# Kernel tuning notes

Hardware: AMD Instinct MI355X
Metric: run time of the kernel (lower is better)

The kernel has to match this reference:

```python
import jax, jax.numpy as jnp
import numpy as np

N_NODES = 50000
N_EDGES = 600000
N_RELS = 500
D = 128


def setup_inputs() -> dict:
    key = jax.random.key(0)
    ks = jax.random.split(key, 8)
    h = jax.random.normal(ks[0], (N_NODES, D), dtype=jnp.float32)
    norm = jax.random.uniform(ks[1], (N_NODES, 1), dtype=jnp.float32)
    rel_emb = jax.random.normal(ks[2], (N_RELS, D), dtype=jnp.float32)
    # xavier-uniform-like scale for square weights
    lim = np.sqrt(6.0 / (D + D)) * np.sqrt(2.0)
    W_neighbor = jax.random.uniform(ks[3], (D, D), dtype=jnp.float32, minval=-lim, maxval=lim)
    loop_weight = jax.random.uniform(ks[4], (D, D), dtype=jnp.float32, minval=-lim, maxval=lim)
    edge_src = jax.random.randint(ks[5], (N_EDGES,), 0, N_NODES, dtype=jnp.int64 if jax.config.jax_enable_x64 else jnp.int32)
    edge_dst = jax.random.randint(ks[6], (N_EDGES,), 0, N_NODES, dtype=edge_src.dtype)
    edge_type = jax.random.randint(ks[7], (N_EDGES,), 0, N_RELS, dtype=edge_src.dtype)
    return {
        "h": h, "norm": norm, "rel_emb": rel_emb,
        "W_neighbor": W_neighbor, "loop_weight": loop_weight,
        "edge_src": edge_src, "edge_dst": edge_dst, "edge_type": edge_type,
    }


def reference(h, norm, rel_emb, W_neighbor, loop_weight, edge_src, edge_dst, edge_type):
    # self-loop message (dense GEMM on node features)
    loop_message = h @ loop_weight  # [N, D]

    # msg_func: gather rel emb + src features, compose ('sub' branch computes node + relation
    # in the original source, reproduced faithfully), dense matmul per edge
    relation = rel_emb[edge_type]          # [E, D] gather
    node = h[edge_src]                     # [E, D] gather
    msg = (node + relation) @ W_neighbor   # [E, D]

    # fn.sum aggregate: scatter-sum messages into destination nodes
    agg = jax.ops.segment_sum(msg, edge_dst, num_segments=h.shape[0])  # [N, D]

    # apply_func: multiply by per-node norm
    node_repr = agg * norm  # [N, D]

    # self_loop add, then activation (relu); dropout=0.0 -> identity
    node_repr = jax.nn.relu(node_repr + loop_message)
    return node_repr
```

## Files before the change

kernel.cpp:

```cpp
#include <hip/hip_runtime.h>

#define NN 50000
#define NE 600000
#define NR 500
#define DD 128
#define CAP 64

#define CSTRIDE 32


#define OFF_CUR  0
#define OFF_BKT  (NN * CSTRIDE)
#define OFF_HB   (OFF_BKT + NN * CAP)
#define OFF_RELB (OFF_HB + NN * DD / 2)
#define OFF_BP   (OFF_RELB + NR * DD / 2)

typedef __bf16 bf16x8 __attribute__((ext_vector_type(8)));
typedef float  f32x4  __attribute__((ext_vector_type(4)));
typedef float  f32x4v __attribute__((ext_vector_type(4)));

#define FILL_BLOCKS ((NE + 255) / 256)
#define HB_BLOCKS   3125
#define RELB_BLOCKS 32
#define PB_BLOCKS   128
#define PREP_BLOCKS (FILL_BLOCKS + HB_BLOCKS + RELB_BLOCKS + PB_BLOCKS)

__global__ __launch_bounds__(256) void prep_fill(
    const float* __restrict__ h, const float* __restrict__ rel,
    const float* __restrict__ W, const float* __restrict__ L,
    __bf16* __restrict__ h_bf, __bf16* __restrict__ rel_bf,
    __bf16* __restrict__ Bp,
    const int* __restrict__ esrc, const int* __restrict__ edst,
    const int* __restrict__ etyp, int* __restrict__ cursor,
    unsigned* __restrict__ bucket)
{
    int b = blockIdx.x;
    if (b < FILL_BLOCKS) {
        int e = b * 256 + threadIdx.x;
        if (e >= NE) return;
        int s = __builtin_nontemporal_load(esrc + e);
        int d = __builtin_nontemporal_load(edst + e);
        int t = __builtin_nontemporal_load(etyp + e);
        int pos = atomicAdd(&cursor[(size_t)d * CSTRIDE], 1);
        if (pos < CAP) bucket[(size_t)d * CAP + pos] = (unsigned)s | ((unsigned)t << 16);
        return;
    }
    b -= FILL_BLOCKS;
    if (b < HB_BLOCKS) {
        int t = b * 256 + threadIdx.x;
        const f32x4v* src = (const f32x4v*)h + (size_t)t * 2;
        f32x4v v0 = __builtin_nontemporal_load(src);
        f32x4v v1 = __builtin_nontemporal_load(src + 1);
        bf16x8 o;
        o[0]=(__bf16)v0[0]; o[1]=(__bf16)v0[1]; o[2]=(__bf16)v0[2]; o[3]=(__bf16)v0[3];
        o[4]=(__bf16)v1[0]; o[5]=(__bf16)v1[1]; o[6]=(__bf16)v1[2]; o[7]=(__bf16)v1[3];
        *(bf16x8*)(h_bf + (size_t)t * 8) = o;
    } else if (b < HB_BLOCKS + RELB_BLOCKS) {
        int t = (b - HB_BLOCKS) * 256 + threadIdx.x;
        if (t < NR * DD / 8) {
            const f32x4v* src = (const f32x4v*)rel + (size_t)t * 2;
            f32x4v v0 = src[0], v1 = src[1];
            bf16x8 o;
            o[0]=(__bf16)v0[0]; o[1]=(__bf16)v0[1]; o[2]=(__bf16)v0[2]; o[3]=(__bf16)v0[3];
            o[4]=(__bf16)v1[0]; o[5]=(__bf16)v1[1]; o[6]=(__bf16)v1[2]; o[7]=(__bf16)v1[3];
            *(bf16x8*)(rel_bf + (size_t)t * 8) = o;
        }
    } else {
        int t = (b - HB_BLOCKS - RELB_BLOCKS) * 256 + threadIdx.x;
        int lane  = (t >> 3) & 63;
        int ntile = (t >> 9) & 7;
        int kstep = t >> 12;
        int n = ntile * 16 + (lane & 15);
        int k = kstep * 32 + (lane >> 4) * 8 + (t & 7);
        float v = (k < DD) ? W[k * DD + n] : L[(k - DD) * DD + n];
        Bp[t] = (__bf16)v;
    }
}

#define AP 264

__global__ __launch_bounds__(256) void fused_gather_mfma(
    const __bf16* __restrict__ h_bf, const __bf16* __restrict__ rel_bf,
    const float* __restrict__ norm, const int* __restrict__ cursor,
    const unsigned* __restrict__ bucket, const __bf16* __restrict__ Bp,
    float* __restrict__ out)
{
    __shared__ __bf16 As[16 * AP];
    int tid = threadIdx.x;
    int row0 = blockIdx.x * 16;
    int g    = tid >> 4;
    int gl   = tid & 15;
    int node = row0 + g;

    bf16x8 own_h = *(const bf16x8*)(h_bf + (size_t)node * DD + gl * 8);
    float sc = norm[node];
    int n = cursor[(size_t)node * CSTRIDE];
    n = (n < CAP) ? n : CAP;
    const unsigned* bk = bucket + (size_t)node * CAP;

    float acc[8];
#pragma unroll
    for (int j = 0; j < 8; ++j) acc[j] = 0.f;

    int i = 0;
    if (n >= 8) {
        unsigned w[8];
#pragma unroll
        for (int u = 0; u < 8; ++u) w[u] = bk[u];
        for (; i + 7 < n; i += 8) {
            bf16x8 a[8], r[8];
#pragma unroll
            for (int u = 0; u < 8; ++u) {
                a[u] = *(const bf16x8*)(h_bf   + (size_t)(w[u] & 0xFFFFu) * DD + gl * 8);
                r[u] = *(const bf16x8*)(rel_bf + (size_t)(w[u] >> 16)     * DD + gl * 8);
            }
            unsigned wn[8];
#pragma unroll
            for (int u = 0; u < 8; ++u) wn[u] = bk[i + 8 + u];
#pragma unroll
            for (int u = 0; u < 8; ++u)
#pragma unroll
                for (int j = 0; j < 8; ++j)
                    acc[j] += (float)a[u][j] + (float)r[u][j];
#pragma unroll
            for (int u = 0; u < 8; ++u) w[u] = wn[u];
        }
    }
    for (; i + 1 < n; i += 2) {
        unsigned p0 = bk[i], p1 = bk[i + 1];
        bf16x8 a0 = *(const bf16x8*)(h_bf   + (size_t)(p0 & 0xFFFFu) * DD + gl * 8);
        bf16x8 b0 = *(const bf16x8*)(rel_bf + (size_t)(p0 >> 16)     * DD + gl * 8);
        bf16x8 a1 = *(const bf16x8*)(h_bf   + (size_t)(p1 & 0xFFFFu) * DD + gl * 8);
        bf16x8 b1 = *(const bf16x8*)(rel_bf + (size_t)(p1 >> 16)     * DD + gl * 8);
#pragma unroll
        for (int j = 0; j < 8; ++j)
            acc[j] += ((float)a0[j] + (float)b0[j]) + ((float)a1[j] + (float)b1[j]);
    }
    if (i < n) {
        unsigned p0 = bk[i];
        bf16x8 a0 = *(const bf16x8*)(h_bf   + (size_t)(p0 & 0xFFFFu) * DD + gl * 8);
        bf16x8 b0 = *(const bf16x8*)(rel_bf + (size_t)(p0 >> 16)     * DD + gl * 8);
#pragma unroll
        for (int j = 0; j < 8; ++j) acc[j] += (float)a0[j] + (float)b0[j];
    }

    bf16x8 o;
#pragma unroll
    for (int j = 0; j < 8; ++j) o[j] = (__bf16)(acc[j] * sc);
    *(bf16x8*)&As[g * AP + gl * 8] = o;
    *(bf16x8*)&As[g * AP + DD + gl * 8] = own_h;
    __syncthreads();

    int lane = tid & 63;
    int wave = tid >> 6;
    int aoff = (lane & 15) * AP + (lane >> 4) * 8;

    f32x4 c0 = (f32x4)0.f, c1 = (f32x4)0.f;
    int nt0 = wave * 2;
#pragma unroll
    for (int kstep = 0; kstep < 8; ++kstep) {
        bf16x8 a = *(const bf16x8*)&As[aoff + kstep * 32];
        const __bf16* bbase = Bp + ((size_t)(kstep * 8 + nt0) * 64 + lane) * 8;
        bf16x8 b0 = *(const bf16x8*)bbase;
        bf16x8 b1 = *(const bf16x8*)(bbase + 64 * 8);
        c0 = __builtin_amdgcn_mfma_f32_16x16x32_bf16(a, b0, c0, 0, 0, 0);
        c1 = __builtin_amdgcn_mfma_f32_16x16x32_bf16(a, b1, c1, 0, 0, 0);
    }

    int quad = lane >> 4;
    int col  = lane & 15;
#pragma unroll
    for (int reg = 0; reg < 4; ++reg) {
        float* op = out + (size_t)(row0 + quad * 4 + reg) * DD + col;
        __builtin_nontemporal_store(fmaxf(c0[reg], 0.f), op + nt0 * 16);
        __builtin_nontemporal_store(fmaxf(c1[reg], 0.f), op + (nt0 + 1) * 16);
    }
}

extern "C" void kernel_launch(void* const* d_in, const int* in_sizes, int n_in,
                              void* d_out, int out_size, void* d_ws, size_t ws_size,
                              hipStream_t stream) {
    const float* h    = (const float*)d_in[0];
    const float* norm = (const float*)d_in[1];
    const float* rel  = (const float*)d_in[2];
    const float* W    = (const float*)d_in[3];
    const float* L    = (const float*)d_in[4];
    const int* esrc   = (const int*)d_in[5];
    const int* edst   = (const int*)d_in[6];
    const int* etyp   = (const int*)d_in[7];
    float* out = (float*)d_out;

    int* ws = (int*)d_ws;
    int* cursor      = ws + OFF_CUR;
    unsigned* bucket = (unsigned*)(ws + OFF_BKT);
    __bf16* h_bf     = (__bf16*)(ws + OFF_HB);
    __bf16* rel_bf   = (__bf16*)(ws + OFF_RELB);
    __bf16* Bp       = (__bf16*)(ws + OFF_BP);

    (void)hipMemsetAsync(cursor, 0, (size_t)NN * CSTRIDE * sizeof(int), stream);
    prep_fill<<<PREP_BLOCKS, 256, 0, stream>>>(h, rel, W, L, h_bf, rel_bf, Bp,
                                               esrc, edst, etyp, cursor, bucket);
    fused_gather_mfma<<<NN / 16, 256, 0, stream>>>(h_bf, rel_bf, norm, cursor,
                                                   bucket, Bp, out);
}
```

Before: 161.6 us.

## Self-reset cursor array in consumer kernel and pad gather tail with zero rows

Moves the per-node cursor counters into a device global array that the gather kernel resets to zero after reading, so the memset launch that cleared it every call is removed. The gather loop is also rewritten into uniform 8-edge batches. Missing slots point at an added zero row of h_bf and rel_bf, which removes the 2-wide and scalar tail loops. The approach relies on the first call seeing a zero-initialised global and on every call completing, and padded slots still issue real loads.

```diff
diff --git a/kernel.cpp b/kernel.cpp
--- a/kernel.cpp
+++ b/kernel.cpp
@@ -8,12 +8,14 @@
 
 #define CSTRIDE 32
 
+__device__ int g_cursor[NN * CSTRIDE];
 
-#define OFF_CUR  0
-#define OFF_BKT  (NN * CSTRIDE)
+#define ZW ((unsigned)NN | ((unsigned)NR << 16))
+
+#define OFF_BKT  0
 #define OFF_HB   (OFF_BKT + NN * CAP)
-#define OFF_RELB (OFF_HB + NN * DD / 2)
-#define OFF_BP   (OFF_RELB + NR * DD / 2)
+#define OFF_RELB (OFF_HB + (NN + 1) * DD / 2)
+#define OFF_BP   (OFF_RELB + (NR + 1) * DD / 2)
 
 typedef __bf16 bf16x8 __attribute__((ext_vector_type(8)));
 typedef float  f32x4  __attribute__((ext_vector_type(4)));
@@ -31,8 +33,7 @@
     __bf16* __restrict__ h_bf, __bf16* __restrict__ rel_bf,
     __bf16* __restrict__ Bp,
     const int* __restrict__ esrc, const int* __restrict__ edst,
-    const int* __restrict__ etyp, int* __restrict__ cursor,
-    unsigned* __restrict__ bucket)
+    const int* __restrict__ etyp, unsigned* __restrict__ bucket)
 {
     int b = blockIdx.x;
     if (b < FILL_BLOCKS) {
@@ -41,7 +42,7 @@
         int s = __builtin_nontemporal_load(esrc + e);
         int d = __builtin_nontemporal_load(edst + e);
         int t = __builtin_nontemporal_load(etyp + e);
-        int pos = atomicAdd(&cursor[(size_t)d * CSTRIDE], 1);
+        int pos = atomicAdd(&g_cursor[(size_t)d * CSTRIDE], 1);
         if (pos < CAP) bucket[(size_t)d * CAP + pos] = (unsigned)s | ((unsigned)t << 16);
         return;
     }
@@ -64,6 +65,18 @@
             o[0]=(__bf16)v0[0]; o[1]=(__bf16)v0[1]; o[2]=(__bf16)v0[2]; o[3]=(__bf16)v0[3];
             o[4]=(__bf16)v1[0]; o[5]=(__bf16)v1[1]; o[6]=(__bf16)v1[2]; o[7]=(__bf16)v1[3];
             *(bf16x8*)(rel_bf + (size_t)t * 8) = o;
+        } else if (t < NR * DD / 8 + 16) {
+            int j = t - NR * DD / 8;
+            bf16x8 z;
+#pragma unroll
+            for (int k = 0; k < 8; ++k) z[k] = (__bf16)0.f;
+            *(bf16x8*)(h_bf + (size_t)NN * DD + j * 8) = z;
+        } else if (t < NR * DD / 8 + 32) {
+            int j = t - NR * DD / 8 - 16;
+            bf16x8 z;
+#pragma unroll
+            for (int k = 0; k < 8; ++k) z[k] = (__bf16)0.f;
+            *(bf16x8*)(rel_bf + (size_t)NR * DD + j * 8) = z;
         }
     } else {
         int t = (b - HB_BLOCKS - RELB_BLOCKS) * 256 + threadIdx.x;
@@ -81,7 +94,7 @@
 
 __global__ __launch_bounds__(256) void fused_gather_mfma(
     const __bf16* __restrict__ h_bf, const __bf16* __restrict__ rel_bf,
-    const float* __restrict__ norm, const int* __restrict__ cursor,
+    const float* __restrict__ norm,
     const unsigned* __restrict__ bucket, const __bf16* __restrict__ Bp,
     float* __restrict__ out)
 {
@@ -92,56 +105,38 @@
     int gl   = tid & 15;
     int node = row0 + g;
 
+    const unsigned* bk = bucket + (size_t)node * CAP;
+    unsigned w[8];
+#pragma unroll
+    for (int u = 0; u < 8; ++u) w[u] = bk[u];
+
+    int n = g_cursor[(size_t)node * CSTRIDE];
+    if (gl == 0) g_cursor[(size_t)node * CSTRIDE] = 0;
     bf16x8 own_h = *(const bf16x8*)(h_bf + (size_t)node * DD + gl * 8);
     float sc = norm[node];
-    int n = cursor[(size_t)node * CSTRIDE];
     n = (n < CAP) ? n : CAP;
-    const unsigned* bk = bucket + (size_t)node * CAP;
 
     float acc[8];
 #pragma unroll
     for (int j = 0; j < 8; ++j) acc[j] = 0.f;
 
-    int i = 0;
-    if (n >= 8) {
-        unsigned w[8];
+    int nb = (n + 7) >> 3;
+    for (int b = 0; b < nb; ++b) {
+        int rem = n - b * 8;
+        bf16x8 a[8], r[8];
 #pragma unroll
-        for (int u = 0; u < 8; ++u) w[u] = bk[u];
-        for (; i + 7 < n; i += 8) {
-            bf16x8 a[8], r[8];
+        for (int u = 0; u < 8; ++u) {
+            unsigned wu = (u < rem) ? w[u] : ZW;
+            a[u] = *(const bf16x8*)(h_bf   + (size_t)(wu & 0xFFFFu) * DD + gl * 8);
+            r[u] = *(const bf16x8*)(rel_bf + (size_t)(wu >> 16)     * DD + gl * 8);
+        }
 #pragma unroll
-            for (int u = 0; u < 8; ++u) {
-                a[u] = *(const bf16x8*)(h_bf   + (size_t)(w[u] & 0xFFFFu) * DD + gl * 8);
-                r[u] = *(const bf16x8*)(rel_bf + (size_t)(w[u] >> 16)     * DD + gl * 8);
-            }
-            unsigned wn[8];
+        for (int u = 0; u < 8; ++u) w[u] = bk[(b + 1) * 8 + u];
 #pragma unroll
-            for (int u = 0; u < 8; ++u) wn[u] = bk[i + 8 + u];
+        for (int u = 0; u < 8; ++u)
 #pragma unroll
-            for (int u = 0; u < 8; ++u)
-#pragma unroll
-                for (int j = 0; j < 8; ++j)
-                    acc[j] += (float)a[u][j] + (float)r[u][j];
-#pragma unroll
-            for (int u = 0; u < 8; ++u) w[u] = wn[u];
-        }
-    }
-    for (; i + 1 < n; i += 2) {
-        unsigned p0 = bk[i], p1 = bk[i + 1];
-        bf16x8 a0 = *(const bf16x8*)(h_bf   + (size_t)(p0 & 0xFFFFu) * DD + gl * 8);
-        bf16x8 b0 = *(const bf16x8*)(rel_bf + (size_t)(p0 >> 16)     * DD + gl * 8);
-        bf16x8 a1 = *(const bf16x8*)(h_bf   + (size_t)(p1 & 0xFFFFu) * DD + gl * 8);
-        bf16x8 b1 = *(const bf16x8*)(rel_bf + (size_t)(p1 >> 16)     * DD + gl * 8);
-#pragma unroll
-        for (int j = 0; j < 8; ++j)
-            acc[j] += ((float)a0[j] + (float)b0[j]) + ((float)a1[j] + (float)b1[j]);
-    }
-    if (i < n) {
-        unsigned p0 = bk[i];
-        bf16x8 a0 = *(const bf16x8*)(h_bf   + (size_t)(p0 & 0xFFFFu) * DD + gl * 8);
-        bf16x8 b0 = *(const bf16x8*)(rel_bf + (size_t)(p0 >> 16)     * DD + gl * 8);
-#pragma unroll
-        for (int j = 0; j < 8; ++j) acc[j] += (float)a0[j] + (float)b0[j];
+            for (int j = 0; j < 8; ++j)
+                acc[j] += (float)a[u][j] + (float)r[u][j];
     }
 
     bf16x8 o;
@@ -191,15 +186,13 @@
     float* out = (float*)d_out;
 
     int* ws = (int*)d_ws;
-    int* cursor      = ws + OFF_CUR;
     unsigned* bucket = (unsigned*)(ws + OFF_BKT);
     __bf16* h_bf     = (__bf16*)(ws + OFF_HB);
     __bf16* rel_bf   = (__bf16*)(ws + OFF_RELB);
     __bf16* Bp       = (__bf16*)(ws + OFF_BP);
 
-    (void)hipMemsetAsync(cursor, 0, (size_t)NN * CSTRIDE * sizeof(int), stream);
     prep_fill<<<PREP_BLOCKS, 256, 0, stream>>>(h, rel, W, L, h_bf, rel_bf, Bp,
-                                               esrc, edst, etyp, cursor, bucket);
-    fused_gather_mfma<<<NN / 16, 256, 0, stream>>>(h_bf, rel_bf, norm, cursor,
+                                               esrc, edst, etyp, bucket);
+    fused_gather_mfma<<<NN / 16, 256, 0, stream>>>(h_bf, rel_bf, norm,
                                                    bucket, Bp, out);
 }
```

Result: faster. 157.3 us (-2.7%).
